# Optimization experiments

Hardware: AMD Instinct MI355X
Metric: run time of the kernel (lower is better)

The kernel has to match this reference:

```python
import jax, jax.numpy as jnp
import numpy as np

NUM_HEADS = 16
HEAD_DIM = 64
HIDDEN = NUM_HEADS * HEAD_DIM  # 1024
SEQ_LEN = 4096


def setup_inputs() -> dict:
    key = jax.random.key(0)
    ks = jax.random.split(key, 8)
    hidden_states = jax.random.normal(ks[0], (SEQ_LEN, HIDDEN), dtype=jnp.float32)
    cu_seqlens = jnp.sort(jax.random.randint(ks[1], (5,), 0, SEQ_LEN)).astype(jnp.int32)
    cos = jax.random.uniform(ks[2], (SEQ_LEN, HEAD_DIM), dtype=jnp.float32)
    sin = jax.random.uniform(ks[3], (SEQ_LEN, HEAD_DIM), dtype=jnp.float32)
    W_qkv = jax.random.normal(ks[4], (HIDDEN, 3 * HIDDEN), dtype=jnp.float32) * 0.02
    b_qkv = jax.random.normal(ks[5], (3 * HIDDEN,), dtype=jnp.float32) * 0.02
    W_proj = jax.random.normal(ks[6], (HIDDEN, HIDDEN), dtype=jnp.float32) * 0.02
    b_proj = jax.random.normal(ks[7], (HIDDEN,), dtype=jnp.float32) * 0.02
    return {
        "hidden_states": hidden_states,
        "cu_seqlens": cu_seqlens,
        "cos": cos,
        "sin": sin,
        "W_qkv": W_qkv,
        "b_qkv": b_qkv,
        "W_proj": W_proj,
        "b_proj": b_proj,
    }


def _rotate_half(x):
    x1, x2 = jnp.split(x, 2, axis=-1)
    return jnp.concatenate([-x2, x1], axis=-1)


def reference(hidden_states, cu_seqlens, cos, sin, W_qkv, b_qkv, W_proj, b_proj):
    # NOTE: original module does not use cu_seqlens for masking (full dense attention).
    seq_len = hidden_states.shape[0]
    qkv = hidden_states @ W_qkv + b_qkv  # (S, 3*H)
    qkv = qkv.reshape(seq_len, 3, NUM_HEADS, HEAD_DIM)
    q, k, v = qkv[:, 0], qkv[:, 1], qkv[:, 2]  # (S, nh, hd)
    c = cos[:, None, :]
    s = sin[:, None, :]
    q = q * c + _rotate_half(q) * s
    k = k * c + _rotate_half(k) * s
    scale = 1.0 / jnp.sqrt(jnp.float32(HEAD_DIM))
    # (nh, S, hd)
    q = q.transpose(1, 0, 2)
    k = k.transpose(1, 0, 2)
    v = v.transpose(1, 0, 2)
    attn = jnp.einsum('hqd,hkd->hqk', q, k) * scale
    attn = jax.nn.softmax(attn, axis=-1)
    out = jnp.einsum('hqk,hkd->hqd', attn, v)
    out = out.transpose(1, 0, 2).reshape(seq_len, HIDDEN)
    return out @ W_proj + b_proj
```

## Files before the change

### kernel.cpp

```cpp
#include <hip/hip_runtime.h>
#include <type_traits>

typedef short bf16x8 __attribute__((ext_vector_type(8)));
typedef float f32x4  __attribute__((ext_vector_type(4)));
typedef unsigned short u16;

#define MFMA(a,b,c) __builtin_amdgcn_mfma_f32_16x16x32_bf16((a),(b),(c),0,0,0)

__device__ __forceinline__ float bf2f(u16 u){ unsigned x=((unsigned)u)<<16; return __builtin_bit_cast(float,x); }
__device__ __forceinline__ u16 f2bf(float f){ unsigned x=__builtin_bit_cast(unsigned,f); x += 0x7fffu + ((x>>16)&1u); return (u16)(x>>16); }

#if __has_builtin(__builtin_amdgcn_cvt_pk_bf16_f32)
typedef __bf16 hwbf2 __attribute__((ext_vector_type(2)));
__device__ __forceinline__ unsigned pkbf(float a, float b){
  hwbf2 r = __builtin_amdgcn_cvt_pk_bf16_f32(a, b);
  return __builtin_bit_cast(unsigned, r);
}
#else
__device__ __forceinline__ unsigned pkbf(float a, float b){
  unsigned ua = __builtin_bit_cast(unsigned, a), ub = __builtin_bit_cast(unsigned, b);
  ua += 0x7fffu + ((ua>>16)&1u);
  ub += 0x7fffu + ((ub>>16)&1u);
  return __builtin_amdgcn_perm(ub, ua, 0x07060302u);
}
#endif

#if __has_builtin(__builtin_amdgcn_exp2f)
#define EXP2(x) __builtin_amdgcn_exp2f(x)
#else
#define EXP2(x) exp2f(x)
#endif

__device__ __forceinline__ void async_cp16(const u16* g, u16* l){
  __builtin_amdgcn_global_load_lds((const __attribute__((address_space(1))) void*)g,
                                   (__attribute__((address_space(3))) void*)l, 16, 0, 0);
}

__global__ __launch_bounds__(256) void cvt_f32_bf16(const float* __restrict__ in, u16* __restrict__ out, int n){
  int i = (blockIdx.x*256 + threadIdx.x)*4;
  if (i >= n) return;
  float4 v = *(const float4*)(in + i);
  ushort4 o;
  o.x = f2bf(v.x); o.y = f2bf(v.y); o.z = f2bf(v.z); o.w = f2bf(v.w);
  *(ushort4*)(out + i) = o;
}

__global__ __launch_bounds__(256) void transpose_f32_bf16(const float* __restrict__ in, u16* __restrict__ out, int R, int C){
  __shared__ u16 tile[32][33];
  int bc = blockIdx.x*32, br = blockIdx.y*32;
  int tx = threadIdx.x & 31, ty = threadIdx.x >> 5;
  #pragma unroll
  for (int i=ty;i<32;i+=8) tile[i][tx] = f2bf(in[(size_t)(br+i)*C + bc + tx]);
  __syncthreads();
  #pragma unroll
  for (int i=ty;i<32;i+=8) out[(size_t)(bc+i)*R + br + tx] = tile[tx][i];
}

__global__ __launch_bounds__(256) void vtrans_perm_bf16(const u16* __restrict__ in, u16* __restrict__ out){
  __shared__ u16 tile[32][33];
  const int h = blockIdx.z;
  const u16* ip = in + (size_t)h*4096*64;
  u16* op = out + (size_t)h*64*4096;
  int bt = blockIdx.x*32, bd = blockIdx.y*32;
  int tx = threadIdx.x & 31, ty = threadIdx.x >> 5;
  #pragma unroll
  for (int i=ty;i<32;i+=8) tile[i][tx] = ip[(size_t)(bt+i)*64 + bd + tx];
  __syncthreads();
  const int tlog = ((tx>>2)&1)*16 + (tx>>3)*4 + (tx&3);
  #pragma unroll
  for (int i=ty;i<32;i+=8) op[(size_t)(bd+i)*4096 + bt + tx] = tile[tlog][i];
}

template<int BN, typename OutT>
__global__ __launch_bounds__(256) void gemm_bt_bias(
    const u16* __restrict__ A, const u16* __restrict__ Bt,
    const float* __restrict__ bias, OutT* __restrict__ C,
    int M, int N, int K)
{
  __shared__ __align__(16) u16 As[128*32];
  __shared__ __align__(16) u16 Bs[BN*32];
  const int m0 = blockIdx.y*128, n0 = blockIdx.x*BN;
  const int tid = threadIdx.x;
  const int wave = tid>>6, lane = tid&63;
  const int wr = (wave>>1)*64, wc = (wave&1)*(BN/2);
  const int ml = lane&15, quad = lane>>4;
  const int lrow = lane>>2;
  const int scol = ((lane&3) ^ (lrow&3))*8;
  const int rsw  = (quad ^ (ml&3))*8;
  const u16* gA0 = A + (size_t)(m0 + wave*32      + lrow)*K + scol;
  const u16* gA1 = A + (size_t)(m0 + wave*32 + 16 + lrow)*K + scol;
  u16* lA0 = &As[wave*1024];
  u16* lA1 = &As[wave*1024 + 512];
  constexpr int BI = BN/64;
  const u16* gB[BI]; u16* lB[BI];
  #pragma unroll
  for (int t=0;t<BI;t++){
    gB[t] = Bt + (size_t)(n0 + (wave*BI+t)*16 + lrow)*K + scol;
    lB[t] = &Bs[(wave*BI+t)*512];
  }
  constexpr int NJ = BN/32;
  f32x4 acc[4][NJ] = {};
  for (int k0=0; k0<K; k0+=32) {
    async_cp16(gA0 + k0, lA0);
    async_cp16(gA1 + k0, lA1);
    #pragma unroll
    for (int t=0;t<BI;t++) async_cp16(gB[t] + k0, lB[t]);
    __syncthreads();
    bf16x8 af[4], bfr[NJ];
    #pragma unroll
    for (int i=0;i<4;i++)  af[i]  = *(const bf16x8*)&As[(wr+i*16+ml)*32 + rsw];
    #pragma unroll
    for (int j=0;j<NJ;j++) bfr[j] = *(const bf16x8*)&Bs[(wc+j*16+ml)*32 + rsw];
    #pragma unroll
    for (int i=0;i<4;i++)
      #pragma unroll
      for (int j=0;j<NJ;j++)
        acc[i][j] = MFMA(af[i], bfr[j], acc[i][j]);
    __syncthreads();
  }
  #pragma unroll
  for (int j=0;j<NJ;j++){
    int col = n0 + wc + j*16 + ml;
    float bv = bias[col];
    #pragma unroll
    for (int i=0;i<4;i++){
      int row0 = m0 + wr + i*16 + quad*4;
      #pragma unroll
      for (int r=0;r<4;r++){
        float val = acc[i][j][r] + bv;
        if constexpr (std::is_same_v<OutT, float>)
          C[(size_t)(row0+r)*N + col] = val;
        else
          C[(size_t)(row0+r)*N + col] = f2bf(val);
      }
    }
  }
}

__global__ __launch_bounds__(256) void rope_split(
    const u16* __restrict__ QKV, const float* __restrict__ cosb, const float* __restrict__ sinb,
    u16* __restrict__ Qo, u16* __restrict__ Ko, u16* __restrict__ Vo)
{
  const int t = blockIdx.x;
  const int d = threadIdx.x & 63;
  const int h0 = threadIdx.x >> 6;
  const float cv = cosb[t*64+d];
  const float sv = sinb[t*64+d];
  const int dp = (d<32) ? d+32 : d-32;
  const float sgn = (d<32) ? -1.f : 1.f;
  #pragma unroll
  for (int h=h0; h<16; h+=4) {
    const u16* base = QKV + (size_t)t*3072 + h*64;
    float q  = bf2f(base[d]);
    float k  = bf2f(base[1024+d]);
    float v  = bf2f(base[2048+d]);
    float qp = bf2f(base[dp]);
    float kp = bf2f(base[1024+dp]);
    float qr = q*cv + sgn*qp*sv;
    float kr = k*cv + sgn*kp*sv;
    Qo[((size_t)h*4096 + t)*64 + d] = f2bf(qr*(0.125f*1.44269504f));
    Ko[((size_t)h*4096 + t)*64 + d] = f2bf(kr);
    Vo[((size_t)h*4096 + t)*64 + d] = f2bf(v);
  }
}

__global__ __launch_bounds__(256,4) void flash_attn(
    const u16* __restrict__ Q, const u16* __restrict__ Kg, const u16* __restrict__ VT,
    u16* __restrict__ O0, u16* __restrict__ O1, u16* __restrict__ O2, u16* __restrict__ O3,
    float* __restrict__ Lpart)
{
  constexpr int SEQ=4096, QTR=1024;
  __shared__ __align__(16) u16 Ks[64*64];
  __shared__ __align__(16) u16 Vs[64*64];
  const int qt=blockIdx.x, h=blockIdx.y, ks=blockIdx.z;
  const int tid=threadIdx.x, wave=tid>>6, lane=tid&63;
  const int ml=lane&15, quad=lane>>4;
  const int qbase = qt*128 + wave*32;
  bf16x8 qf[2][2];
  #pragma unroll
  for (int qi=0; qi<2; qi++){
    const u16* qp = Q + ((size_t)h*SEQ + qbase + qi*16 + ml)*64;
    qf[qi][0] = *(const bf16x8*)(qp + quad*8);
    qf[qi][1] = *(const bf16x8*)(qp + 32 + quad*8);
  }
  const bf16x8 ones = {0x3F80,0x3F80,0x3F80,0x3F80,0x3F80,0x3F80,0x3F80,0x3F80};
  f32x4 o[2][4] = {};
  f32x4 accsum[2] = {};
  const int lrow8 = lane>>3, lchk = lane&7;
  const int swzg = (lchk ^ lrow8)*8;
  const u16* kgl = Kg + (size_t)h*SEQ*64 + (size_t)(ks*QTR + wave*16 + lrow8)*64 + swzg;
  const u16* vgl = VT + (size_t)h*64*SEQ + (size_t)(wave*16 + lrow8)*SEQ + ks*QTR + swzg;
  u16* kl0 = &Ks[(wave*16  )*64];
  u16* kl1 = &Ks[(wave*16+8)*64];
  u16* vl0 = &Vs[(wave*16  )*64];
  u16* vl1 = &Vs[(wave*16+8)*64];
  const int swzA = (quad     ^ (ml&7))*8;
  const int swzB = ((quad^4) ^ (ml&7))*8;

  for (int k0=0;k0<QTR;k0+=64) {
    async_cp16(kgl + (size_t)k0*64,       kl0);
    async_cp16(kgl + (size_t)k0*64 + 512, kl1);
    async_cp16(vgl + k0,                  vl0);
    async_cp16(vgl + 8*SEQ + k0,          vl1);
    __syncthreads();
    f32x4 s[2][4];
    #pragma unroll
    for (int kb=0;kb<4;kb++){
      bf16x8 kf0 = *(const bf16x8*)&Ks[(kb*16+ml)*64 + swzA];
      bf16x8 kf1 = *(const bf16x8*)&Ks[(kb*16+ml)*64 + swzB];
      f32x4 z0={0,0,0,0}, z1={0,0,0,0};
      z0 = MFMA(kf0, qf[0][0], z0); s[0][kb] = MFMA(kf1, qf[0][1], z0);
      z1 = MFMA(kf0, qf[1][0], z1); s[1][kb] = MFMA(kf1, qf[1][1], z1);
    }
    bf16x8 vf[4][2];
    #pragma unroll
    for (int db=0;db<4;db++){
      vf[db][0] = *(const bf16x8*)&Vs[(db*16+ml)*64 + swzA];
      vf[db][1] = *(const bf16x8*)&Vs[(db*16+ml)*64 + swzB];
    }
    #pragma unroll
    for (int qi=0; qi<2; qi++)
      #pragma unroll
      for (int p=0;p<2;p++){
        float e0 = EXP2(s[qi][2*p][0]),   e1 = EXP2(s[qi][2*p][1]);
        float e2 = EXP2(s[qi][2*p][2]),   e3 = EXP2(s[qi][2*p][3]);
        float e4 = EXP2(s[qi][2*p+1][0]), e5 = EXP2(s[qi][2*p+1][1]);
        float e6 = EXP2(s[qi][2*p+1][2]), e7 = EXP2(s[qi][2*p+1][3]);
        union { uint4 u; bf16x8 v; } pf;
        pf.u.x = pkbf(e0,e1); pf.u.y = pkbf(e2,e3);
        pf.u.z = pkbf(e4,e5); pf.u.w = pkbf(e6,e7);
        accsum[qi] = MFMA(ones, pf.v, accsum[qi]);
        #pragma unroll
        for (int db=0;db<4;db++)
          o[qi][db] = MFMA(vf[db][p], pf.v, o[qi][db]);
      }
    __syncthreads();
  }
  u16* op = (ks==0) ? O0 : (ks==1) ? O1 : (ks==2) ? O2 : O3;
  #pragma unroll
  for (int qi=0;qi<2;qi++){
    size_t rb = (size_t)(qbase + qi*16 + ml)*1024 + h*64;
    #pragma unroll
    for (int db=0;db<4;db++){
      uint2 w;
      w.x = pkbf(o[qi][db][0], o[qi][db][1]);
      w.y = pkbf(o[qi][db][2], o[qi][db][3]);
      *(uint2*)&op[rb + db*16 + quad*4] = w;
    }
  }
  if (quad==0){
    float* lp = Lpart + (size_t)ks*65536 + (size_t)h*4096 + qbase;
    lp[ml]    = accsum[0][0];
    lp[16+ml] = accsum[1][0];
  }
}

__global__ __launch_bounds__(256) void combine_softmax4(
    const u16* __restrict__ O0, const u16* __restrict__ O1,
    const u16* __restrict__ O2, const u16* __restrict__ O3,
    const float* __restrict__ L, u16* __restrict__ AO)
{
  int i = (blockIdx.x*256 + threadIdx.x)*4;
  int row = i >> 10, col = i & 1023, h = col >> 6;
  int li = h*4096 + row;
  float inv = 1.f/(L[li] + L[li+65536] + L[li+2*65536] + L[li+3*65536]);
  ushort4 a = *(const ushort4*)(O0+i);
  ushort4 b = *(const ushort4*)(O1+i);
  ushort4 c = *(const ushort4*)(O2+i);
  ushort4 d = *(const ushort4*)(O3+i);
  ushort4 o;
  o.x = f2bf((bf2f(a.x)+bf2f(b.x)+bf2f(c.x)+bf2f(d.x))*inv);
  o.y = f2bf((bf2f(a.y)+bf2f(b.y)+bf2f(c.y)+bf2f(d.y))*inv);
  o.z = f2bf((bf2f(a.z)+bf2f(b.z)+bf2f(c.z)+bf2f(d.z))*inv);
  o.w = f2bf((bf2f(a.w)+bf2f(b.w)+bf2f(c.w)+bf2f(d.w))*inv);
  *(ushort4*)(AO+i) = o;
}

extern "C" void kernel_launch(void* const* d_in, const int* in_sizes, int n_in,
                              void* d_out, int out_size, void* d_ws, size_t ws_size,
                              hipStream_t stream)
{
  (void)in_sizes; (void)n_in; (void)out_size; (void)ws_size;
  const float* H     = (const float*)d_in[0];
  const float* cosb  = (const float*)d_in[2];
  const float* sinb  = (const float*)d_in[3];
  const float* Wqkv  = (const float*)d_in[4];
  const float* bqkv  = (const float*)d_in[5];
  const float* Wproj = (const float*)d_in[6];
  const float* bproj = (const float*)d_in[7];
  float* out = (float*)d_out;
  char* ws = (char*)d_ws;
  float* Lpart  = (float*)(ws + 0);
  u16*   WprojT = (u16*)(ws + 2097152);
  u16*   Hb     = (u16*)(ws + 4194304);
  u16*   Opart2 = (u16*)(ws + 4194304);
  u16*   QKVr   = (u16*)(ws + 12582912);
  u16*   VTb    = (u16*)(ws + 12582912);
  u16*   Opart0 = (u16*)(ws + 20971520);
  u16*   Opart1 = (u16*)(ws + 29360128);
  u16*   WqkvT  = (u16*)(ws + 37748736);
  u16*   Qb     = (u16*)(ws + 37748736);
  u16*   AO     = (u16*)(ws + 37748736);
  u16*   Kb     = (u16*)(ws + 46137344);
  u16*   Vb     = (u16*)(ws + 54525952);
  u16*   Opart3 = (u16*)(ws + 54525952);

  hipLaunchKernelGGL(cvt_f32_bf16, dim3(4096), dim3(256), 0, stream, H, Hb, 4096*1024);
  hipLaunchKernelGGL(transpose_f32_bf16, dim3(96,32), dim3(256), 0, stream, Wqkv, WqkvT, 1024, 3072);
  hipLaunchKernelGGL(transpose_f32_bf16, dim3(32,32), dim3(256), 0, stream, Wproj, WprojT, 1024, 1024);
  hipLaunchKernelGGL((gemm_bt_bias<128,u16>), dim3(24,32), dim3(256), 0, stream, Hb, WqkvT, bqkv, QKVr, 4096, 3072, 1024);
  hipLaunchKernelGGL(rope_split, dim3(4096), dim3(256), 0, stream, QKVr, cosb, sinb, Qb, Kb, Vb);
  hipLaunchKernelGGL(vtrans_perm_bf16, dim3(128,2,16), dim3(256), 0, stream, Vb, VTb);
  hipLaunchKernelGGL(flash_attn, dim3(32,16,4), dim3(256), 0, stream, Qb, Kb, VTb,
                     Opart0, Opart1, Opart2, Opart3, Lpart);
  hipLaunchKernelGGL(combine_softmax4, dim3(4096), dim3(256), 0, stream,
                     Opart0, Opart1, Opart2, Opart3, Lpart, AO);
  hipLaunchKernelGGL((gemm_bt_bias<64,float>), dim3(16,32), dim3(256), 0, stream, AO, WprojT, bproj, out, 4096, 1024, 1024);
}
```

Baseline: 256.3 us.

## Fuse RoPE into QKV GEMM epilogue, merge prep kernels, deepen GEMM K tile

Combines the H conversion and both weight transposes into one prep kernel launch. The QKV GEMM now applies bias, RoPE, Q scaling and the head-split scatter in its epilogue, which removes the intermediate QKV buffer and the separate rope_split pass. It pairs each column with its rotate-half partner from the accumulator held in the same thread. Both GEMMs move from a K-step of 32 to 64 with an 8-chunk XOR swizzle, halving the number of barrier iterations at the cost of twice the LDS. Workspace offsets are reshuffled to fit the new buffer lifetimes.

```diff
diff --git a/kernel.cpp b/kernel.cpp
--- a/kernel.cpp
+++ b/kernel.cpp
@@ -36,24 +36,117 @@
                                    (__attribute__((address_space(3))) void*)l, 16, 0, 0);
 }
 
-__global__ __launch_bounds__(256) void cvt_f32_bf16(const float* __restrict__ in, u16* __restrict__ out, int n){
-  int i = (blockIdx.x*256 + threadIdx.x)*4;
-  if (i >= n) return;
-  float4 v = *(const float4*)(in + i);
-  ushort4 o;
-  o.x = f2bf(v.x); o.y = f2bf(v.y); o.z = f2bf(v.z); o.w = f2bf(v.w);
-  *(ushort4*)(out + i) = o;
-}
-
-__global__ __launch_bounds__(256) void transpose_f32_bf16(const float* __restrict__ in, u16* __restrict__ out, int R, int C){
+__global__ __launch_bounds__(256) void prep(
+    const float* __restrict__ H, const float* __restrict__ Wqkv, const float* __restrict__ Wproj,
+    u16* __restrict__ Hb, u16* __restrict__ WqkvT, u16* __restrict__ WprojT)
+{
   __shared__ u16 tile[32][33];
-  int bc = blockIdx.x*32, br = blockIdx.y*32;
-  int tx = threadIdx.x & 31, ty = threadIdx.x >> 5;
+  const int bid = blockIdx.x, tid = threadIdx.x;
+  if (bid < 4096) {
+    int i = (bid*256 + tid)*4;
+    float4 v = *(const float4*)(H + i);
+    ushort4 o;
+    o.x = f2bf(v.x); o.y = f2bf(v.y); o.z = f2bf(v.z); o.w = f2bf(v.w);
+    *(ushort4*)(Hb + i) = o;
+    return;
+  }
+  const float* in; u16* out; int R, C, bx, by;
+  if (bid < 7168) { int t = bid-4096; in=Wqkv; out=WqkvT; R=1024; C=3072; bx=t%96; by=t/96; }
+  else            { int t = bid-7168; in=Wproj; out=WprojT; R=1024; C=1024; bx=t%32; by=t/32; }
+  int bc = bx*32, br = by*32;
+  int tx = tid & 31, ty = tid >> 5;
   #pragma unroll
   for (int i=ty;i<32;i+=8) tile[i][tx] = f2bf(in[(size_t)(br+i)*C + bc + tx]);
   __syncthreads();
   #pragma unroll
   for (int i=ty;i<32;i+=8) out[(size_t)(bc+i)*R + br + tx] = tile[tx][i];
+}
+
+__global__ __launch_bounds__(256) void gemm_qkv_rope(
+    const u16* __restrict__ A, const u16* __restrict__ Bt,
+    const float* __restrict__ bias, const float* __restrict__ cosb, const float* __restrict__ sinb,
+    u16* __restrict__ Qo, u16* __restrict__ Ko, u16* __restrict__ Vo)
+{
+  constexpr int K = 1024;
+  __shared__ __align__(16) u16 As[128*64];
+  __shared__ __align__(16) u16 Bs[128*64];
+  const int m0 = blockIdx.y*128, n0 = blockIdx.x*128;
+  const int tid = threadIdx.x, wave = tid>>6, lane = tid&63;
+  const int wr = (wave>>1)*64, wc = (wave&1)*64;
+  const int ml = lane&15, quad = lane>>4;
+  const int lrow8 = lane>>3, lchk = lane&7;
+  const int swzg = (lchk ^ lrow8)*8;
+  const u16* gA[4]; u16* lA[4];
+  const u16* gB[4]; u16* lB[4];
+  #pragma unroll
+  for (int t=0;t<4;t++){
+    gA[t] = A  + (size_t)(m0 + wave*32 + t*8 + lrow8)*K + swzg;
+    lA[t] = &As[(wave*32 + t*8)*64];
+    gB[t] = Bt + (size_t)(n0 + wave*32 + t*8 + lrow8)*K + swzg;
+    lB[t] = &Bs[(wave*32 + t*8)*64];
+  }
+  f32x4 acc[4][4] = {};
+  const int rch0 = ( quad     ^ (ml&7))*8;
+  const int rch1 = ((quad|4) ^ (ml&7))*8;
+  for (int k0=0; k0<K; k0+=64) {
+    #pragma unroll
+    for (int t=0;t<4;t++){ async_cp16(gA[t]+k0, lA[t]); async_cp16(gB[t]+k0, lB[t]); }
+    __syncthreads();
+    #pragma unroll
+    for (int kk=0;kk<2;kk++){
+      const int rc = kk ? rch1 : rch0;
+      bf16x8 af[4], bfr[4];
+      #pragma unroll
+      for (int i=0;i<4;i++)  af[i]  = *(const bf16x8*)&As[(wr+i*16+ml)*64 + rc];
+      #pragma unroll
+      for (int j=0;j<4;j++) bfr[j] = *(const bf16x8*)&Bs[(wc+j*16+ml)*64 + rc];
+      #pragma unroll
+      for (int i=0;i<4;i++)
+        #pragma unroll
+        for (int j=0;j<4;j++)
+          acc[i][j] = MFMA(af[i], bfr[j], acc[i][j]);
+    }
+    __syncthreads();
+  }
+  const int region = n0 >> 10;
+  if (region == 2) {
+    #pragma unroll
+    for (int j=0;j<4;j++){
+      int col = n0 + wc + j*16 + ml;
+      int dloc = col & 63, hh = (col & 1023) >> 6;
+      float bv = bias[col];
+      #pragma unroll
+      for (int i=0;i<4;i++){
+        int row0 = m0 + wr + i*16 + quad*4;
+        #pragma unroll
+        for (int r=0;r<4;r++)
+          Vo[((size_t)hh*4096 + row0 + r)*64 + dloc] = f2bf(acc[i][j][r] + bv);
+      }
+    }
+  } else {
+    u16* dst = region ? Ko : Qo;
+    const float qs = region ? 1.0f : 0.125f*1.44269504f;
+    #pragma unroll
+    for (int j=0;j<4;j++){
+      int col = n0 + wc + j*16 + ml;
+      int dloc = col & 63, hh = (col & 1023) >> 6;
+      float bv  = bias[col];
+      float bvp = bias[col ^ 32];
+      float sgn = (dloc < 32) ? -1.f : 1.f;
+      #pragma unroll
+      for (int i=0;i<4;i++){
+        int row0 = m0 + wr + i*16 + quad*4;
+        #pragma unroll
+        for (int r=0;r<4;r++){
+          int t = row0 + r;
+          float c = cosb[t*64 + dloc], s = sinb[t*64 + dloc];
+          float val = acc[i][j][r]   + bv;
+          float par = acc[i][j^2][r] + bvp;
+          dst[((size_t)hh*4096 + t)*64 + dloc] = f2bf((val*c + sgn*par*s)*qs);
+        }
+      }
+    }
+  }
 }
 
 __global__ __launch_bounds__(256) void vtrans_perm_bf16(const u16* __restrict__ in, u16* __restrict__ out){
@@ -77,45 +170,51 @@
     const float* __restrict__ bias, OutT* __restrict__ C,
     int M, int N, int K)
 {
-  __shared__ __align__(16) u16 As[128*32];
-  __shared__ __align__(16) u16 Bs[BN*32];
+  __shared__ __align__(16) u16 As[128*64];
+  __shared__ __align__(16) u16 Bs[BN*64];
   const int m0 = blockIdx.y*128, n0 = blockIdx.x*BN;
-  const int tid = threadIdx.x;
-  const int wave = tid>>6, lane = tid&63;
+  const int tid = threadIdx.x, wave = tid>>6, lane = tid&63;
   const int wr = (wave>>1)*64, wc = (wave&1)*(BN/2);
   const int ml = lane&15, quad = lane>>4;
-  const int lrow = lane>>2;
-  const int scol = ((lane&3) ^ (lrow&3))*8;
-  const int rsw  = (quad ^ (ml&3))*8;
-  const u16* gA0 = A + (size_t)(m0 + wave*32      + lrow)*K + scol;
-  const u16* gA1 = A + (size_t)(m0 + wave*32 + 16 + lrow)*K + scol;
-  u16* lA0 = &As[wave*1024];
-  u16* lA1 = &As[wave*1024 + 512];
-  constexpr int BI = BN/64;
+  const int lrow8 = lane>>3, lchk = lane&7;
+  const int swzg = (lchk ^ lrow8)*8;
+  const u16* gA[4]; u16* lA[4];
+  #pragma unroll
+  for (int t=0;t<4;t++){
+    gA[t] = A + (size_t)(m0 + wave*32 + t*8 + lrow8)*K + swzg;
+    lA[t] = &As[(wave*32 + t*8)*64];
+  }
+  constexpr int BI = BN/32;
   const u16* gB[BI]; u16* lB[BI];
   #pragma unroll
   for (int t=0;t<BI;t++){
-    gB[t] = Bt + (size_t)(n0 + (wave*BI+t)*16 + lrow)*K + scol;
-    lB[t] = &Bs[(wave*BI+t)*512];
+    gB[t] = Bt + (size_t)(n0 + wave*(BN/4) + t*8 + lrow8)*K + swzg;
+    lB[t] = &Bs[(wave*(BN/4) + t*8)*64];
   }
   constexpr int NJ = BN/32;
   f32x4 acc[4][NJ] = {};
-  for (int k0=0; k0<K; k0+=32) {
-    async_cp16(gA0 + k0, lA0);
-    async_cp16(gA1 + k0, lA1);
-    #pragma unroll
-    for (int t=0;t<BI;t++) async_cp16(gB[t] + k0, lB[t]);
-    __syncthreads();
-    bf16x8 af[4], bfr[NJ];
-    #pragma unroll
-    for (int i=0;i<4;i++)  af[i]  = *(const bf16x8*)&As[(wr+i*16+ml)*32 + rsw];
-    #pragma unroll
-    for (int j=0;j<NJ;j++) bfr[j] = *(const bf16x8*)&Bs[(wc+j*16+ml)*32 + rsw];
-    #pragma unroll
-    for (int i=0;i<4;i++)
-      #pragma unroll
-      for (int j=0;j<NJ;j++)
-        acc[i][j] = MFMA(af[i], bfr[j], acc[i][j]);
+  const int rch0 = ( quad     ^ (ml&7))*8;
+  const int rch1 = ((quad|4) ^ (ml&7))*8;
+  for (int k0=0; k0<K; k0+=64) {
+    #pragma unroll
+    for (int t=0;t<4;t++)  async_cp16(gA[t]+k0, lA[t]);
+    #pragma unroll
+    for (int t=0;t<BI;t++) async_cp16(gB[t]+k0, lB[t]);
+    __syncthreads();
+    #pragma unroll
+    for (int kk=0;kk<2;kk++){
+      const int rc = kk ? rch1 : rch0;
+      bf16x8 af[4], bfr[NJ];
+      #pragma unroll
+      for (int i=0;i<4;i++)  af[i]  = *(const bf16x8*)&As[(wr+i*16+ml)*64 + rc];
+      #pragma unroll
+      for (int j=0;j<NJ;j++) bfr[j] = *(const bf16x8*)&Bs[(wc+j*16+ml)*64 + rc];
+      #pragma unroll
+      for (int i=0;i<4;i++)
+        #pragma unroll
+        for (int j=0;j<NJ;j++)
+          acc[i][j] = MFMA(af[i], bfr[j], acc[i][j]);
+    }
     __syncthreads();
   }
   #pragma unroll
@@ -134,33 +233,6 @@
           C[(size_t)(row0+r)*N + col] = f2bf(val);
       }
     }
-  }
-}
-
-__global__ __launch_bounds__(256) void rope_split(
-    const u16* __restrict__ QKV, const float* __restrict__ cosb, const float* __restrict__ sinb,
-    u16* __restrict__ Qo, u16* __restrict__ Ko, u16* __restrict__ Vo)
-{
-  const int t = blockIdx.x;
-  const int d = threadIdx.x & 63;
-  const int h0 = threadIdx.x >> 6;
-  const float cv = cosb[t*64+d];
-  const float sv = sinb[t*64+d];
-  const int dp = (d<32) ? d+32 : d-32;
-  const float sgn = (d<32) ? -1.f : 1.f;
-  #pragma unroll
-  for (int h=h0; h<16; h+=4) {
-    const u16* base = QKV + (size_t)t*3072 + h*64;
-    float q  = bf2f(base[d]);
-    float k  = bf2f(base[1024+d]);
-    float v  = bf2f(base[2048+d]);
-    float qp = bf2f(base[dp]);
-    float kp = bf2f(base[1024+dp]);
-    float qr = q*cv + sgn*qp*sv;
-    float kr = k*cv + sgn*kp*sv;
-    Qo[((size_t)h*4096 + t)*64 + d] = f2bf(qr*(0.125f*1.44269504f));
-    Ko[((size_t)h*4096 + t)*64 + d] = f2bf(kr);
-    Vo[((size_t)h*4096 + t)*64 + d] = f2bf(v);
   }
 }
 
@@ -194,7 +266,7 @@
   u16* kl1 = &Ks[(wave*16+8)*64];
   u16* vl0 = &Vs[(wave*16  )*64];
   u16* vl1 = &Vs[(wave*16+8)*64];
-  const int swzA = (quad     ^ (ml&7))*8;
+  const int swzA = ( quad     ^ (ml&7))*8;
   const int swzB = ((quad^4) ^ (ml&7))*8;
 
   for (int k0=0;k0<QTR;k0+=64) {
@@ -293,27 +365,25 @@
   float* Lpart  = (float*)(ws + 0);
   u16*   WprojT = (u16*)(ws + 2097152);
   u16*   Hb     = (u16*)(ws + 4194304);
-  u16*   Opart2 = (u16*)(ws + 4194304);
-  u16*   QKVr   = (u16*)(ws + 12582912);
-  u16*   VTb    = (u16*)(ws + 12582912);
-  u16*   Opart0 = (u16*)(ws + 20971520);
-  u16*   Opart1 = (u16*)(ws + 29360128);
+  u16*   VTb    = (u16*)(ws + 4194304);
+  u16*   Qb     = (u16*)(ws + 12582912);
+  u16*   AO     = (u16*)(ws + 12582912);
+  u16*   Kb     = (u16*)(ws + 20971520);
+  u16*   Vb     = (u16*)(ws + 29360128);
+  u16*   Opart3 = (u16*)(ws + 29360128);
   u16*   WqkvT  = (u16*)(ws + 37748736);
-  u16*   Qb     = (u16*)(ws + 37748736);
-  u16*   AO     = (u16*)(ws + 37748736);
-  u16*   Kb     = (u16*)(ws + 46137344);
-  u16*   Vb     = (u16*)(ws + 54525952);
-  u16*   Opart3 = (u16*)(ws + 54525952);
-
-  hipLaunchKernelGGL(cvt_f32_bf16, dim3(4096), dim3(256), 0, stream, H, Hb, 4096*1024);
-  hipLaunchKernelGGL(transpose_f32_bf16, dim3(96,32), dim3(256), 0, stream, Wqkv, WqkvT, 1024, 3072);
-  hipLaunchKernelGGL(transpose_f32_bf16, dim3(32,32), dim3(256), 0, stream, Wproj, WprojT, 1024, 1024);
-  hipLaunchKernelGGL((gemm_bt_bias<128,u16>), dim3(24,32), dim3(256), 0, stream, Hb, WqkvT, bqkv, QKVr, 4096, 3072, 1024);
-  hipLaunchKernelGGL(rope_split, dim3(4096), dim3(256), 0, stream, QKVr, cosb, sinb, Qb, Kb, Vb);
+  u16*   Opart0 = (u16*)(ws + 37748736);
+  u16*   Opart1 = (u16*)(ws + 46137344);
+  u16*   Opart2 = (u16*)(ws + 54525952);
+
+  hipLaunchKernelGGL(prep, dim3(8192), dim3(256), 0, stream, H, Wqkv, Wproj, Hb, WqkvT, WprojT);
+  hipLaunchKernelGGL(gemm_qkv_rope, dim3(24,32), dim3(256), 0, stream,
+                     Hb, WqkvT, bqkv, cosb, sinb, Qb, Kb, Vb);
   hipLaunchKernelGGL(vtrans_perm_bf16, dim3(128,2,16), dim3(256), 0, stream, Vb, VTb);
   hipLaunchKernelGGL(flash_attn, dim3(32,16,4), dim3(256), 0, stream, Qb, Kb, VTb,
                      Opart0, Opart1, Opart2, Opart3, Lpart);
   hipLaunchKernelGGL(combine_softmax4, dim3(4096), dim3(256), 0, stream,
                      Opart0, Opart1, Opart2, Opart3, Lpart, AO);
-  hipLaunchKernelGGL((gemm_bt_bias<64,float>), dim3(16,32), dim3(256), 0, stream, AO, WprojT, bproj, out, 4096, 1024, 1024);
-}
+  hipLaunchKernelGGL((gemm_bt_bias<64,float>), dim3(16,32), dim3(256), 0, stream,
+                     AO, WprojT, bproj, out, 4096, 1024, 1024);
+}
```

Result: no change. 251.8 us (-1.7%).
